# Performance work log

Measured on AMD Instinct MI355X. Metric: run time of the kernel, lower is better.

## Reference

```python
import jax, jax.numpy as jnp
import numpy as np
jax.config.update("jax_enable_x64", True)  # int64 hash codes for lattice keys

N_KPTS = 32768
C = 61      # feature channels; f-MLP input dim is C+3 = 64
D = 64      # disp-distribution channels
D_LAT = 8   # last f-layer output -> permutohedral position dim

# large odd 62-bit multipliers for the lattice-key hash (wraps mod 2^64)
_MULTS = np.array([2654435761405764093, 1181783497276652981,
                   3202034522624059733, 2685821657736338717,
                   1876998521354586173, 1481765933965188213,
                   2549297995355413921, 3373259426345127233], dtype=np.int64)


def _hcode(k, mults):
    return jnp.sum(k.astype(jnp.int64) * mults, axis=-1)


def _pl_filter(pos, vals):
    """Permutohedral lattice splat -> blur -> slice (approx. Gaussian filter).
    pos: (N, d) float32 lattice positions, vals: (N, vd) float32 values."""
    N, d = pos.shape
    vd = vals.shape[1]
    M = N * (d + 1)  # fixed-size hash table (every point touches d+1 vertices)
    # --- elevate onto hyperplane H_d in R^{d+1} ---
    scale = np.float32(np.sqrt(2.0 / 3.0) * (d + 1)) / np.sqrt(
        np.arange(1, d + 1, dtype=np.float32) * np.arange(2, d + 2, dtype=np.float32))
    E = np.zeros((d + 1, d), dtype=np.float32)
    E[0, :] = 1.0
    for i in range(1, d + 1):
        E[i, i - 1] = -float(i)
        E[i, i:] = 1.0
    elevated = (pos * jnp.asarray(scale, jnp.float32)) @ jnp.asarray(E).T  # (N, d+1)
    # --- nearest zero-colored lattice point and simplex ranks ---
    rem0 = jnp.floor(elevated / (d + 1) + 0.5) * (d + 1)
    sum_val = jnp.round(jnp.sum(rem0, -1) / (d + 1)).astype(jnp.int32)
    diff = elevated - rem0
    rank = jnp.argsort(jnp.argsort(-diff, axis=-1), axis=-1).astype(jnp.int32) + sum_val[:, None]
    lo = rank < 0
    hi = rank > d
    rem0 = rem0 + jnp.where(lo, float(d + 1), 0.0) - jnp.where(hi, float(d + 1), 0.0)
    rank = rank + jnp.where(lo, d + 1, 0) - jnp.where(hi, d + 1, 0)
    # --- barycentric coordinates ---
    t = (elevated - rem0) / (d + 1)
    rows = jnp.arange(N)[:, None]
    bary = jnp.zeros((N, d + 2), jnp.float32)
    bary = bary.at[rows, d - rank].add(t)
    bary = bary.at[rows, d + 1 - rank].add(-t)
    bary = bary.at[:, 0].add(1.0 + bary[:, d + 1])
    w = bary[:, :d + 1]  # (N, d+1) vertex weights
    # --- simplex vertex keys (first d coords; full key sums to 0) ---
    canonical = np.zeros((d + 1, d + 1), np.int32)
    for r in range(d + 1):
        canonical[r, :d + 1 - r] = r
        canonical[r, d + 1 - r:] = r - (d + 1)
    keys = rem0.astype(jnp.int32)[None, :, :d] + jnp.asarray(canonical)[:, rank[:, :d]]  # (d+1,N,d)
    # --- hash table via sorted unique codes (jit-safe fixed size) ---
    mults = jnp.asarray(_MULTS[:d])
    codes = _hcode(keys, mults).reshape(M)
    uniq, inv = jnp.unique(codes, return_inverse=True, size=M,
                           fill_value=jnp.iinfo(jnp.int64).max)
    inv = inv.reshape(M)
    # --- splat ---
    wv = (w.T[:, :, None] * vals[None]).reshape(M, vd)
    lat = jax.ops.segment_sum(wv, inv, num_segments=M)  # (M, vd)
    occ = jax.ops.segment_sum(jnp.ones((M,), jnp.float32), inv, num_segments=M) > 0
    ukeys = jnp.zeros((M, d), jnp.int32).at[inv].set(keys.reshape(M, d))
    # --- blur along each of the d+1 lattice directions ---
    for j in range(d + 1):
        off = np.ones(d + 1, np.int32)
        off[j] = -d
        o = jnp.asarray(off[:d])
        def _nbr(sign, lat=lat):
            c = _hcode(ukeys + sign * o, mults)
            i = jnp.clip(jnp.searchsorted(uniq, c), 0, M - 1)
            ok = (jnp.take(uniq, i) == c) & jnp.take(occ, i)
            return jnp.where(ok[:, None], jnp.take(lat, i, axis=0), 0.0)
        lat = jnp.where(occ[:, None], 0.5 * lat + 0.25 * (_nbr(1) + _nbr(-1)), lat)
    # --- slice ---
    alpha = 1.0 / (1.0 + 2.0 ** (-d))
    return jnp.sum(w.T[:, :, None] * jnp.take(lat, inv, axis=0).reshape(d + 1, N, vd), 0) * alpha


def _layernorm2(x, g, b):
    # LayerNorm(normalized_shape=(N, K)): stats over the last TWO dims jointly
    mu = jnp.mean(x, axis=(-2, -1), keepdims=True)
    var = jnp.mean((x - mu) ** 2, axis=(-2, -1), keepdims=True)
    return (x - mu) * jax.lax.rsqrt(var + 1e-5) * g + b


def setup_inputs() -> dict:
    key = jax.random.key(0)
    ks = jax.random.split(key, 16)
    f32 = jnp.float32
    rn = lambda k, shape, s=1.0: jax.random.normal(k, shape, dtype=f32) * s
    inp = {
        "kpts": rn(ks[0], (1, N_KPTS, 3)),
        "disps_distr": rn(ks[1], (1, N_KPTS, D)),
        "feats": rn(ks[2], (1, N_KPTS, C)),
    }
    i = 3
    for b in range(2):
        inp[f"Wd{b}0"] = rn(ks[i], (D, D), 0.05); i += 1
        inp[f"bd{b}0"] = jnp.zeros((D,), f32)
        inp[f"Wd{b}1"] = rn(ks[i], (D, D), 0.05); i += 1
        inp[f"bd{b}1"] = jnp.zeros((D,), f32)
        inp[f"Wf{b}"] = rn(ks[i], (C + 3, D_LAT), 0.1); i += 1
        inp[f"bf{b}"] = jnp.zeros((D_LAT,), f32)
        inp[f"g{b}"] = jnp.ones((N_KPTS, D_LAT), f32)
        inp[f"be{b}"] = jnp.zeros((N_KPTS, D_LAT), f32)
    return inp


def reference(kpts, disps_distr, feats, Wd00, bd00, Wd01, bd01, Wf0, bf0, g0, be0,
              Wd10, bd10, Wd11, bd11, Wf1, bf1, g1, be1):
    fk = jnp.concatenate([kpts, feats], axis=-1)  # (1, N, C+3)
    x = jnp.reshape(disps_distr, (1, N_KPTS, -1))
    blocks = [(Wd00, bd00, Wd01, bd01, Wf0, bf0, g0, be0),
              (Wd10, bd10, Wd11, bd11, Wf1, bf1, g1, be1)]
    for (Wd0, bd0, Wd1, bd1, Wf, bf, g, be) in blocks:
        x = jax.nn.relu(x @ Wd0 + bd0)   # d-layer 0
        x = jax.nn.relu(x @ Wd1 + bd1)   # d-layer 1
        # only the LAST f-layer output is used by the torch code (feats_kpts is never updated)
        pos = _layernorm2(jax.nn.relu(fk @ Wf + bf), g, be)  # (1, N, 8)
        x = _pl_filter(pos[0], x[0])[None]
    return x
```

## Files before the change

### kernel.cpp

```cpp
#include <hip/hip_runtime.h>
#include <hip/hip_bf16.h>
#include <hip/hip_fp16.h>
#include <stdint.h>

typedef unsigned long long u64;

#define NK 32768
#define DL 8
#define DP1 9
#define MT (NK*DP1)
#define HBITS 19
#define HSIZE (1u<<HBITS)
#define HMASK (HSIZE-1)
#define EMPTY_CODE 0xFFFFFFFFFFFFFFFFULL
#define NBLK 1152
#define HBLK (HSIZE/256)
#define CAP 32
#define MAXHUB 16384

#define MLPB 512
#define POSB (NK/32)
#define EMBB (NK/256)
#define HZB  384
#define VZB  128
#define NBRB (9*MT/256)
#define SPAB (MT/8)
#define SPBB 1152

__device__ __constant__ u64 c_mults[8] = {
    2654435761405764093ULL, 1181783497276652981ULL, 3202034522624059733ULL,
    2685821657736338717ULL, 1876998521354586173ULL, 1481765933965188213ULL,
    2549297995355413921ULL, 3373259426345127233ULL};

__device__ __forceinline__ unsigned int hmix(u64 x) {
    return (unsigned int)(x >> (64 - HBITS)) & HMASK;
}

__device__ __forceinline__ u64 dir_delta(int j) {
    u64 s = 0;
    #pragma unroll
    for (int k = 0; k < 8; k++) s += c_mults[k];
    return (j == 8) ? s : (s - 9ULL * c_mults[j]);
}

__device__ __forceinline__ float ldf(const void* p, int i, int bf) {
    if (bf) return __bfloat162float(((const __hip_bfloat16*)p)[i]);
    return ((const float*)p)[i];
}

__device__ __forceinline__ float bf2f(unsigned short u) {
    union { unsigned u; float f; } c; c.u = ((unsigned)u) << 16; return c.f;
}

__device__ __forceinline__ float4 ld4(const void* p, int vi, int bf) {
    if (bf) {
        ushort4 u = ((const ushort4*)p)[vi];
        float4 r;
        r.x = bf2f(u.x); r.y = bf2f(u.y); r.z = bf2f(u.z); r.w = bf2f(u.w);
        return r;
    }
    return ((const float4*)p)[vi];
}

__device__ __forceinline__ float rdlane(float v, int k) {
    return __uint_as_float(__builtin_amdgcn_readlane(__float_as_uint(v), k));
}

__global__ void k_detect(const unsigned* __restrict__ g0w, int* __restrict__ flag,
                         double* __restrict__ stats) {
    if (threadIdx.x == 0) {
        int f = 1;
        for (int i = 0; i < 8; i++) if (g0w[i] != 0x3F803F80u) f = 0;
        *flag = f;
        stats[0] = 0.0; stats[1] = 0.0;
    }
}

__global__ __launch_bounds__(256) void k_mlppos(const void* __restrict__ xin, int use_df_in,
    const void* __restrict__ W0, const void* __restrict__ B0,
    const void* __restrict__ W1, const void* __restrict__ B1,
    float* __restrict__ xout, const int* __restrict__ df,
    const void* __restrict__ kpts, const void* __restrict__ feats,
    const void* __restrict__ Wf, const void* __restrict__ Bf,
    float* __restrict__ pos_pre, double* __restrict__ stats) {
    __shared__ union {
        struct { float w0[4096], w1[4096]; } m;
        struct { float wf[512]; float fk[32][65]; float red[256], red2[256]; } p;
    } sm;
    int bf = *df;
    int tid = threadIdx.x;
    if (blockIdx.x < MLPB) {
        int bfin = use_df_in ? bf : 0;
        for (int i = tid; i < 1024; i += 256) {
            ((float4*)sm.m.w0)[i] = ld4(W0, i, bf);
            ((float4*)sm.m.w1)[i] = ld4(W1, i, bf);
        }
        __syncthreads();
        int lane = tid & 63, wv = tid >> 6;
        float b0c = ldf(B0, lane, bf);
        float b1c = ldf(B1, lane, bf);
        for (int t = 0; t < 2; t++) {
            int row0 = (blockIdx.x * 2 + t) * 32 + wv * 8;
            float a[8], acc[8];
            #pragma unroll
            for (int r = 0; r < 8; r++) {
                a[r] = ldf(xin, (row0 + r) * 64 + lane, bfin);
                acc[r] = b0c;
            }
            #pragma unroll 8
            for (int k = 0; k < 64; k++) {
                float w = sm.m.w0[k * 64 + lane];
                #pragma unroll
                for (int r = 0; r < 8; r++)
                    acc[r] = fmaf(rdlane(a[r], k), w, acc[r]);
            }
            #pragma unroll
            for (int r = 0; r < 8; r++) { a[r] = fmaxf(acc[r], 0.f); acc[r] = b1c; }
            #pragma unroll 8
            for (int k = 0; k < 64; k++) {
                float w = sm.m.w1[k * 64 + lane];
                #pragma unroll
                for (int r = 0; r < 8; r++)
                    acc[r] = fmaf(rdlane(a[r], k), w, acc[r]);
            }
            #pragma unroll
            for (int r = 0; r < 8; r++)
                xout[(row0 + r) * 64 + lane] = fmaxf(acc[r], 0.f);
        }
    } else {
        int n0 = (blockIdx.x - MLPB) * 32;
        for (int i = tid; i < 512; i += 256) sm.p.wf[i] = ldf(Wf, i, bf);
        for (int i = tid; i < 32*64; i += 256) {
            int pt = i >> 6, k = i & 63, n = n0 + pt;
            sm.p.fk[pt][k] = (k < 3) ? ldf(kpts, n*3 + k, bf) : ldf(feats, n*61 + (k-3), bf);
        }
        __syncthreads();
        int pt = tid >> 3, j = tid & 7, n = n0 + pt;
        float acc = ldf(Bf, j, bf);
        #pragma unroll
        for (int k = 0; k < 64; k++) acc = fmaf(sm.p.fk[pt][k], sm.p.wf[k*8+j], acc);
        acc = fmaxf(acc, 0.f);
        pos_pre[n*8 + j] = acc;
        sm.p.red[tid] = acc; sm.p.red2[tid] = acc * acc;
        __syncthreads();
        for (int s = 128; s > 0; s >>= 1) {
            if (tid < s) { sm.p.red[tid] += sm.p.red[tid+s]; sm.p.red2[tid] += sm.p.red2[tid+s]; }
            __syncthreads();
        }
        if (tid == 0) { atomicAdd(&stats[0], (double)sm.p.red[0]); atomicAdd(&stats[1], (double)sm.p.red2[0]); }
    }
}

__global__ __launch_bounds__(256) void k_embedz(const float* __restrict__ pos_pre,
    const double* __restrict__ stats, const void* __restrict__ g,
    const void* __restrict__ be, float* __restrict__ wgt,
    u64* __restrict__ pcodes, int* __restrict__ cnt, int* __restrict__ cnt2,
    int* __restrict__ hubid, const int* __restrict__ df,
    u64* __restrict__ htabc, float* __restrict__ hubval) {
    int bid = blockIdx.x;
    if (bid >= EMBB) {
        if (bid < EMBB + HZB) {
            uint4 f; f.x = 0xFFFFFFFFu; f.y = 0xFFFFFFFFu; f.z = 0xFFFFFFFFu; f.w = 0xFFFFFFFFu;
            for (int i = (bid - EMBB) * 256 + threadIdx.x; i < (int)(HSIZE/2); i += HZB * 256)
                ((uint4*)htabc)[i] = f;
        } else {
            uint4 z; z.x = 0; z.y = 0; z.z = 0; z.w = 0;
            for (int i = (bid - EMBB - HZB) * 256 + threadIdx.x; i < MAXHUB*16; i += VZB * 256)
                ((uint4*)hubval)[i] = z;
        }
        return;
    }
    int bf = *df;
    int n = bid * 256 + threadIdx.x;
    if (n >= NK) return;
    const double inv_cnt = 1.0 / (double)(NK * DL);
    double mud = stats[0] * inv_cnt;
    double vard = stats[1] * inv_cnt - mud * mud;
    float mu = (float)mud;
    float rs = rsqrtf((float)vard + 1e-5f);
    const float scale[8] = {
        5.196152422706632f, 3.0f, 2.1213203435596424f, 1.643167672515498f,
        1.3416407864998738f, 1.1338934190276817f, 0.9819805060619657f, 0.8660254037844386f};
    float c[8];
    #pragma unroll
    for (int k = 0; k < 8; k++) {
        float v = pos_pre[n*8 + k];
        float p = (v - mu) * rs * ldf(g, n*8 + k, bf) + ldf(be, n*8 + k, bf);
        c[k] = p * scale[k];
    }
    float sufa[9]; sufa[8] = 0.f;
    #pragma unroll
    for (int k = 7; k >= 0; k--) sufa[k] = sufa[k+1] + c[k];
    float elev[9];
    elev[0] = sufa[0];
    #pragma unroll
    for (int i = 1; i < 9; i++) elev[i] = sufa[i] - (float)i * c[i-1];
    int ri[9], sumv = 0;
    float diff[9];
    #pragma unroll
    for (int i = 0; i < 9; i++) {
        ri[i] = (int)floorf(elev[i] / 9.0f + 0.5f);
        sumv += ri[i];
        diff[i] = elev[i] - 9.f * (float)ri[i];
    }
    int rank[9];
    #pragma unroll
    for (int i = 0; i < 9; i++) {
        int r = 0;
        #pragma unroll
        for (int j = 0; j < 9; j++)
            r += (diff[j] > diff[i]) || ((diff[j] == diff[i]) && (j < i));
        rank[i] = r + sumv;
    }
    #pragma unroll
    for (int i = 0; i < 9; i++) {
        if (rank[i] < 0)      { rank[i] += 9; ri[i] += 1; }
        else if (rank[i] > 8) { rank[i] -= 9; ri[i] -= 1; }
    }
    float t[9];
    #pragma unroll
    for (int i = 0; i < 9; i++) t[i] = (elev[i] - 9.f * (float)ri[i]) / 9.f;
    float bary[10];
    #pragma unroll
    for (int i = 0; i < 10; i++) bary[i] = 0.f;
    #pragma unroll
    for (int i = 0; i < 9; i++) { bary[8 - rank[i]] += t[i]; bary[9 - rank[i]] -= t[i]; }
    bary[0] += 1.f + bary[9];
    for (int r = 0; r < 9; r++) {
        u64 code = 0;
        #pragma unroll
        for (int k = 0; k < 8; k++) {
            int key = 9 * ri[k] + ((rank[k] <= 8 - r) ? r : (r - 9));
            code += (u64)(long long)key * c_mults[k];
        }
        int m = n * 9 + r;
        wgt[m] = bary[r];
        pcodes[m] = code;
        cnt[m] = 0;
        cnt2[m] = 0;
        hubid[m] = -1;
    }
}

__global__ __launch_bounds__(256) void k_insert(const u64* __restrict__ pcodes,
    u64* __restrict__ htab_code, unsigned int* __restrict__ ppos) {
    int m = blockIdx.x * 256 + threadIdx.x;
    if (m >= MT) return;
    u64 code = pcodes[m];
    unsigned int pos = hmix(code);
    for (;;) {
        u64 cc = htab_code[pos];
        if (cc == code) break;
        if (cc == EMPTY_CODE) {
            u64 old = atomicCAS(&htab_code[pos], EMPTY_CODE, code);
            if (old == EMPTY_CODE || old == code) break;
        }
        pos = (pos + 1) & HMASK;
    }
    ppos[m] = pos;
}

__global__ __launch_bounds__(256) void k_occ(const u64* __restrict__ htab_code,
    int* __restrict__ bocc) {
    __shared__ int wcnt[4];
    unsigned int i = blockIdx.x * 256 + threadIdx.x;
    bool occ = (htab_code[i] != EMPTY_CODE);
    u64 mask = __ballot(occ);
    int lane = threadIdx.x & 63;
    if (lane == 0) wcnt[threadIdx.x >> 6] = __popcll(mask);
    __syncthreads();
    if (threadIdx.x == 0) bocc[blockIdx.x] = wcnt[0] + wcnt[1] + wcnt[2] + wcnt[3];
}

__global__ __launch_bounds__(256) void k_occscan(int* __restrict__ bocc,
    int* __restrict__ counter, int* __restrict__ nhub) {
    __shared__ int s[256];
    __shared__ int carry;
    int t = threadIdx.x;
    if (t == 0) { carry = 0; *nhub = 0; }
    __syncthreads();
    for (int c = 0; c < HBLK / 256; c++) {
        int i = c * 256 + t;
        int v = bocc[i];
        s[t] = v; __syncthreads();
        for (int off = 1; off < 256; off <<= 1) {
            int a = (t >= off) ? s[t-off] : 0;
            __syncthreads();
            s[t] += a;
            __syncthreads();
        }
        int cl = carry;
        bocc[i] = s[t] - v + cl;
        __syncthreads();
        if (t == 0) carry = cl + s[255];
        __syncthreads();
    }
    if (t == 0) *counter = carry;
}

__global__ __launch_bounds__(256) void k_assign2(const u64* __restrict__ htab_code,
    const int* __restrict__ bocc, int* __restrict__ htab_slot,
    u64* __restrict__ slot_code) {
    __shared__ int wbase[4];
    unsigned int i = blockIdx.x * 256 + threadIdx.x;
    u64 cde = htab_code[i];
    bool occ = (cde != EMPTY_CODE);
    int lane = threadIdx.x & 63;
    int wid  = threadIdx.x >> 6;
    u64 mask = __ballot(occ);
    int prefix = __popcll(mask & ((1ULL << lane) - 1ULL));
    if (lane == 0) wbase[wid] = __popcll(mask);
    __syncthreads();
    if (threadIdx.x == 0) {
        int run = bocc[blockIdx.x];
        for (int w = 0; w < 4; w++) { int c = wbase[w]; wbase[w] = run; run += c; }
    }
    __syncthreads();
    if (occ) {
        int s = wbase[wid] + prefix;
        htab_slot[i] = s;
        slot_code[s] = cde;
    }
}

__global__ __launch_bounds__(256) void k_nbrlookup(const u64* __restrict__ slot_code,
    const u64* __restrict__ htab_code, const int* __restrict__ htab_slot,
    const int* __restrict__ counter, int2* __restrict__ nbr,
    const unsigned int* __restrict__ ppos, int* __restrict__ sidx,
    int* __restrict__ cnt) {
    if (blockIdx.x < NBRB) {
        int idx = blockIdx.x * 256 + threadIdx.x;
        int j = idx / MT;
        int sl = idx - j * MT;
        int count = *counter;
        if (sl >= count) return;
        u64 dj = dir_delta(j);
        u64 code = slot_code[sl];
        int res[2];
        #pragma unroll
        for (int s = 0; s < 2; s++) {
            u64 cde = code + (s ? (u64)(0ULL - dj) : dj);
            unsigned int pos = hmix(cde);
            int r = -1;
            for (;;) {
                u64 cc = htab_code[pos];
                if (cc == cde) { r = htab_slot[pos]; break; }
                if (cc == EMPTY_CODE) break;
                pos = (pos + 1) & HMASK;
            }
            res[s] = r;
        }
        nbr[j * MT + sl] = make_int2(res[0], res[1]);
    } else {
        int m = (blockIdx.x - NBRB) * 256 + threadIdx.x;
        if (m >= MT) return;
        int s = htab_slot[ppos[m]];
        sidx[m] = s;
        atomicAdd(&cnt[s], 1);
    }
}

__global__ __launch_bounds__(256) void k_scan1(const int* __restrict__ cnt,
    int* __restrict__ exbuf, int* __restrict__ bsum,
    int* __restrict__ hublist, int* __restrict__ hubid, int* __restrict__ nhub) {
    __shared__ int s[256];
    int t = threadIdx.x;
    int i = blockIdx.x * 256 + t;
    int v = cnt[i];
    if (v > CAP) {
        int h = atomicAdd(nhub, 1);
        if (h < MAXHUB) { hublist[h] = i; hubid[i] = h; }
    }
    s[t] = v; __syncthreads();
    for (int off = 1; off < 256; off <<= 1) {
        int a = (t >= off) ? s[t-off] : 0;
        __syncthreads();
        s[t] += a;
        __syncthreads();
    }
    exbuf[i] = s[t] - v;
    if (t == 255) bsum[blockIdx.x] = s[255];
}

__global__ __launch_bounds__(256) void k_scan2(int* __restrict__ bsum) {
    __shared__ int s[256];
    __shared__ int carry;
    int t = threadIdx.x;
    if (t == 0) carry = 0;
    __syncthreads();
    for (int c = 0; c < (NBLK + 255) / 256; c++) {
        int i = c * 256 + t;
        int v = (i < NBLK) ? bsum[i] : 0;
        s[t] = v; __syncthreads();
        for (int off = 1; off < 256; off <<= 1) {
            int a = (t >= off) ? s[t-off] : 0;
            __syncthreads();
            s[t] += a;
            __syncthreads();
        }
        int cl = carry;
        if (i < NBLK) bsum[i] = s[t] - v + cl;
        __syncthreads();
        if (t == 0) carry = cl + s[255];
        __syncthreads();
    }
}

__global__ __launch_bounds__(256) void k_scatter(const int* __restrict__ sidx,
    const int* __restrict__ exbuf, const int* __restrict__ bsum,
    int* __restrict__ cnt2, int* __restrict__ list) {
    int m = blockIdx.x * 256 + threadIdx.x;
    if (m < MT) {
        int s = sidx[m];
        int ofs = atomicAdd(&cnt2[s], 1);
        list[exbuf[s] + bsum[s >> 8] + ofs] = m;
    }
}

__global__ __launch_bounds__(256) void k_splat(const float* __restrict__ xbuf,
    const float* __restrict__ wgt, const int* __restrict__ exbuf,
    const int* __restrict__ bsum, const int* __restrict__ cnt,
    const int* __restrict__ list, __half* __restrict__ val,
    const int* __restrict__ counter, const int* __restrict__ sidx,
    const int* __restrict__ hubid, float* __restrict__ hubval) {
    const float2* x2 = (const float2*)xbuf;
    int lane = threadIdx.x & 31;
    if (blockIdx.x < SPAB) {
        int count = *counter;
        int sl = blockIdx.x * 8 + (threadIdx.x >> 5);
        if (sl >= count) return;
        int c = cnt[sl];
        if (c > CAP) return;
        int st = exbuf[sl] + bsum[sl >> 8];
        float2 acc = make_float2(0.f, 0.f);
        int mm = 0; float ww = 0.f;
        if (lane < c) { mm = list[st + lane]; ww = wgt[mm]; }
        for (int k = 0; k < c; k++) {
            int   m = __shfl(mm, k, 32);
            float w = __shfl(ww, k, 32);
            float2 xv = x2[(m / 9) * 32 + lane];
            acc.x = fmaf(w, xv.x, acc.x);
            acc.y = fmaf(w, xv.y, acc.y);
        }
        ((__half2*)val)[(size_t)sl * 32 + lane] = __float22half2_rn(acc);
    } else {
        int chunk = (blockIdx.x - SPAB) * 8 + (threadIdx.x >> 5);
        int e = chunk * 32 + lane;
        int m = 0, hid = -1; float w = 0.f; int hub = 0;
        if (e < MT) {
            m = list[e];
            int slot = sidx[m];
            hub = (cnt[slot] > CAP);
            if (hub) { w = wgt[m]; hid = hubid[slot]; }
        }
        u64 bal = __ballot(hub);
        unsigned int half = (threadIdx.x & 32) ? (unsigned int)(bal >> 32) : (unsigned int)bal;
        if (!half) return;
        float2 acc = make_float2(0.f, 0.f);
        int cur = -1;
        while (half) {
            int k = __ffs(half) - 1; half &= half - 1;
            int   hk = __shfl(hid, k, 32);
            int   mk = __shfl(m, k, 32);
            float wk = __shfl(w, k, 32);
            float2 xv = x2[(mk / 9) * 32 + lane];
            if (hk != cur) {
                if (cur >= 0) {
                    atomicAdd(&hubval[(size_t)cur * 64 + 2*lane    ], acc.x);
                    atomicAdd(&hubval[(size_t)cur * 64 + 2*lane + 1], acc.y);
                }
                cur = hk; acc = make_float2(0.f, 0.f);
            }
            acc.x = fmaf(wk, xv.x, acc.x);
            acc.y = fmaf(wk, xv.y, acc.y);
        }
        atomicAdd(&hubval[(size_t)cur * 64 + 2*lane    ], acc.x);
        atomicAdd(&hubval[(size_t)cur * 64 + 2*lane + 1], acc.y);
    }
}

__global__ __launch_bounds__(256) void k_hubcvt(const float* __restrict__ hubval,
    const int* __restrict__ hublist, const int* __restrict__ nhub,
    __half* __restrict__ val) {
    int idx = blockIdx.x * 256 + threadIdx.x;
    int hi = idx >> 5, lane = idx & 31;
    if (hi >= *nhub) return;
    int sl = hublist[hi];
    float2 v = ((const float2*)hubval)[(size_t)hi * 32 + lane];
    ((__half2*)val)[(size_t)sl * 32 + lane] = __float22half2_rn(v);
}

__global__ __launch_bounds__(256) void k_blur(const __half* __restrict__ vin,
    __half* __restrict__ vout, const int2* __restrict__ nbrj,
    const int* __restrict__ counter) {
    int idx = blockIdx.x * 256 + threadIdx.x;
    int sl = idx >> 3, lane = idx & 7;
    int count = *counter;
    if (sl >= count) return;
    int2 nbp = nbrj[sl];
    typedef union { uint4 u; __half2 h[4]; } row16;
    const uint4* vin4 = (const uint4*)vin;
    uint4* vout4 = (uint4*)vout;
    row16 S, A, B, O;
    S.u = vin4[(size_t)sl*8 + lane];
    uint4 z; z.x = 0; z.y = 0; z.z = 0; z.w = 0;
    A.u = (nbp.x >= 0) ? vin4[(size_t)nbp.x*8 + lane] : z;
    B.u = (nbp.y >= 0) ? vin4[(size_t)nbp.y*8 + lane] : z;
    #pragma unroll
    for (int k = 0; k < 4; k++) {
        float2 fs = __half22float2(S.h[k]);
        float2 fa = __half22float2(A.h[k]);
        float2 fb = __half22float2(B.h[k]);
        float2 r;
        r.x = 0.5f * fs.x + 0.25f * (fa.x + fb.x);
        r.y = 0.5f * fs.y + 0.25f * (fa.y + fb.y);
        O.h[k] = __float22half2_rn(r);
    }
    vout4[(size_t)sl*8 + lane] = O.u;
}

__global__ __launch_bounds__(256) void k_slice(const float* __restrict__ wgt,
    const int* __restrict__ sidx, const __half* __restrict__ val,
    float* __restrict__ outf, void* __restrict__ outb, int write_out,
    const int* __restrict__ df, double* __restrict__ stats) {
    int idx = blockIdx.x * 256 + threadIdx.x;
    if (idx == 0) { stats[0] = 0.0; stats[1] = 0.0; }
    if (idx >= NK * 32) return;
    int bf = *df;
    const __half2* v2 = (const __half2*)val;
    int n = idx >> 5, cp = idx & 31;
    float2 acc = make_float2(0.f, 0.f);
    #pragma unroll
    for (int r = 0; r < 9; r++) {
        int m = n * 9 + r;
        float w = wgt[m];
        float2 hv = __half22float2(v2[(size_t)sidx[m]*32 + cp]);
        acc.x = fmaf(w, hv.x, acc.x);
        acc.y = fmaf(w, hv.y, acc.y);
    }
    acc.x *= 0.9961089494163424f;
    acc.y *= 0.9961089494163424f;
    int o = n*64 + cp*2;
    if (write_out) {
        if (bf) {
            __hip_bfloat16* ob = (__hip_bfloat16*)outb;
            ob[o]   = __float2bfloat16(acc.x);
            ob[o+1] = __float2bfloat16(acc.y);
        } else {
            float* of = (float*)outb;
            of[o] = acc.x; of[o+1] = acc.y;
        }
    } else {
        outf[o] = acc.x; outf[o+1] = acc.y;
    }
}

extern "C" void kernel_launch(void* const* d_in, const int* in_sizes, int n_in,
                              void* d_out, int out_size, void* d_ws, size_t ws_size,
                              hipStream_t stream) {
    const void* kpts  = d_in[0];
    const void* disps = d_in[1];
    const void* feats = d_in[2];

    char* p = (char*)d_ws;
    float* xbuf     = (float*)p;  p += (size_t)NK*64*4;
    float* pos_pre  = (float*)p;  p += (size_t)NK*8*4;
    double* stats   = (double*)p; p += 256;
    int*   dflag    = (int*)p;    p += 256;
    float* wgt      = (float*)p;  p += (size_t)MT*4;
    int*   sidx     = (int*)p;    p += (size_t)MT*4;
    u64*   pcodes   = (u64*)p;    p += (size_t)MT*8;
    unsigned int* ppos = (unsigned int*)p; p += (size_t)MT*4;
    u64*   htabc    = (u64*)p;    p += (size_t)HSIZE*8;
    int*   htabs    = (int*)p;    p += (size_t)HSIZE*4;
    u64*   slotc    = (u64*)p;    p += (size_t)MT*8;
    int*   counter  = (int*)p;    p += 256;
    int*   nhub     = (int*)p;    p += 256;
    int*   bocc     = (int*)p;    p += (size_t)HBLK*4;
    int*   cnt      = (int*)p;    p += (size_t)MT*4;
    int*   cnt2     = (int*)p;    p += (size_t)MT*4;
    int*   hubid    = (int*)p;    p += (size_t)MT*4;
    int*   exbuf    = (int*)p;    p += (size_t)MT*4;
    int*   list     = (int*)p;    p += (size_t)MT*4;
    int*   bsum     = (int*)p;    p += 256*32;
    int*   hublist  = (int*)p;    p += (size_t)MAXHUB*4;
    float* hubval   = (float*)p;  p += (size_t)MAXHUB*64*4;
    int2*  nbr      = (int2*)p;   p += (size_t)MT*9*8;
    __half* valA    = (__half*)p; p += (size_t)MT*64*2;
    __half* valB    = (__half*)p; p += (size_t)MT*64*2;

    k_detect<<<1, 64, 0, stream>>>((const unsigned*)d_in[3 + 6], dflag, stats);

    for (int b = 0; b < 2; b++) {
        const void* W0 = d_in[3 + b*8 + 0];
        const void* B0 = d_in[3 + b*8 + 1];
        const void* W1 = d_in[3 + b*8 + 2];
        const void* B1 = d_in[3 + b*8 + 3];
        const void* Wf = d_in[3 + b*8 + 4];
        const void* Bf = d_in[3 + b*8 + 5];
        const void* G  = d_in[3 + b*8 + 6];
        const void* Be = d_in[3 + b*8 + 7];

        k_mlppos<<<MLPB + POSB, 256, 0, stream>>>(
            b == 0 ? disps : (const void*)xbuf, b == 0 ? 1 : 0,
            W0, B0, W1, B1, xbuf, dflag,
            kpts, feats, Wf, Bf, pos_pre, stats);

        k_embedz<<<EMBB + HZB + VZB, 256, 0, stream>>>(pos_pre, stats, G, Be, wgt,
                                                       pcodes, cnt, cnt2, hubid, dflag,
                                                       htabc, hubval);
        k_insert<<<NBLK, 256, 0, stream>>>(pcodes, htabc, ppos);
        k_occ<<<HBLK, 256, 0, stream>>>(htabc, bocc);
        k_occscan<<<1, 256, 0, stream>>>(bocc, counter, nhub);
        k_assign2<<<HBLK, 256, 0, stream>>>(htabc, bocc, htabs, slotc);
        k_nbrlookup<<<NBRB + NBLK, 256, 0, stream>>>(slotc, htabc, htabs, counter, nbr,
                                                     ppos, sidx, cnt);

        k_scan1<<<NBLK, 256, 0, stream>>>(cnt, exbuf, bsum, hublist, hubid, nhub);
        k_scan2<<<1, 256, 0, stream>>>(bsum);
        k_scatter<<<NBLK, 256, 0, stream>>>(sidx, exbuf, bsum, cnt2, list);
        k_splat<<<SPAB + SPBB, 256, 0, stream>>>(xbuf, wgt, exbuf, bsum, cnt, list,
                                                 valA, counter, sidx, hubid, hubval);
        k_hubcvt<<<(MAXHUB*32)/256, 256, 0, stream>>>(hubval, hublist, nhub, valA);

        for (int j = 0; j < 9; j++) {
            const __half* vin = (j & 1) ? valB : valA;
            __half*       vout = (j & 1) ? valA : valB;
            k_blur<<<(MT*8 + 255)/256, 256, 0, stream>>>(vin, vout, nbr + (size_t)j*MT, counter);
        }
        k_slice<<<(NK*64)/256, 256, 0, stream>>>(wgt, sidx, valB, xbuf,
                                                 d_out, b == 1 ? 1 : 0, dflag, stats);
    }
}
```

Before: 710.4 us.

## Register-tile the disparity MLP and split it from the position kernel

The fused MLP/position kernel is split into two launches. The MLP now stages a 64-row input tile in shared memory, and each thread computes 32 output channels for one row using float4 weight reads. This replaces the old scheme, where each lane produced one channel for 8 rows via readlane broadcasts. The aim is more FMAs per shared-memory load and no scalar readlane serialization, at the cost of more registers and shared memory per block, an extra launch, and losing the concurrency the fused grid gave the MLP and position blocks.

```diff
diff --git a/kernel.cpp b/kernel.cpp
--- a/kernel.cpp
+++ b/kernel.cpp
@@ -18,7 +18,7 @@
 #define CAP 32
 #define MAXHUB 16384
 
-#define MLPB 512
+#define MLPGRID (NK/64)
 #define POSB (NK/32)
 #define EMBB (NK/256)
 #define HZB  384
@@ -62,10 +62,6 @@
     return ((const float4*)p)[vi];
 }
 
-__device__ __forceinline__ float rdlane(float v, int k) {
-    return __uint_as_float(__builtin_amdgcn_readlane(__float_as_uint(v), k));
-}
-
 __global__ void k_detect(const unsigned* __restrict__ g0w, int* __restrict__ flag,
                          double* __restrict__ stats) {
     if (threadIdx.x == 0) {
@@ -76,79 +72,102 @@
     }
 }
 
-__global__ __launch_bounds__(256) void k_mlppos(const void* __restrict__ xin, int use_df_in,
+__global__ __launch_bounds__(128) void k_mlp(const void* __restrict__ xin, int use_df_in,
     const void* __restrict__ W0, const void* __restrict__ B0,
     const void* __restrict__ W1, const void* __restrict__ B1,
-    float* __restrict__ xout, const int* __restrict__ df,
-    const void* __restrict__ kpts, const void* __restrict__ feats,
-    const void* __restrict__ Wf, const void* __restrict__ Bf,
-    float* __restrict__ pos_pre, double* __restrict__ stats) {
-    __shared__ union {
-        struct { float w0[4096], w1[4096]; } m;
-        struct { float wf[512]; float fk[32][65]; float red[256], red2[256]; } p;
-    } sm;
+    float* __restrict__ xout, const int* __restrict__ df) {
+    __shared__ float ws0[4096], ws1[4096];
+    __shared__ float xs[64][65];
+    int bf = *df;
+    int bfin = use_df_in ? bf : 0;
+    int tid = threadIdx.x;
+    int lane = tid & 63, wv = tid >> 6;
+    int row0 = blockIdx.x * 64;
+    for (int i = tid; i < 4096; i += 128) {
+        ws0[i] = ldf(W0, i, bf);
+        ws1[i] = ldf(W1, i, bf);
+    }
+    for (int i = tid; i < 1024; i += 128) {
+        int r = i >> 4, kv = i & 15;
+        float4 v = ld4(xin, (row0 + r) * 16 + kv, bfin);
+        xs[r][kv*4  ] = v.x; xs[r][kv*4+1] = v.y;
+        xs[r][kv*4+2] = v.z; xs[r][kv*4+3] = v.w;
+    }
+    __syncthreads();
+    int c0 = wv * 32;
+    float acc[32];
+    #pragma unroll
+    for (int c = 0; c < 32; c++) acc[c] = ldf(B0, c0 + c, bf);
+    for (int k = 0; k < 64; k++) {
+        float xv = xs[lane][k];
+        #pragma unroll
+        for (int c4 = 0; c4 < 8; c4++) {
+            float4 w = *(const float4*)&ws0[k*64 + c0 + c4*4];
+            acc[c4*4  ] = fmaf(xv, w.x, acc[c4*4  ]);
+            acc[c4*4+1] = fmaf(xv, w.y, acc[c4*4+1]);
+            acc[c4*4+2] = fmaf(xv, w.z, acc[c4*4+2]);
+            acc[c4*4+3] = fmaf(xv, w.w, acc[c4*4+3]);
+        }
+    }
+    #pragma unroll
+    for (int c = 0; c < 32; c++) acc[c] = fmaxf(acc[c], 0.f);
+    __syncthreads();
+    #pragma unroll
+    for (int c = 0; c < 32; c++) xs[lane][c0 + c] = acc[c];
+    __syncthreads();
+    #pragma unroll
+    for (int c = 0; c < 32; c++) acc[c] = ldf(B1, c0 + c, bf);
+    for (int k = 0; k < 64; k++) {
+        float xv = xs[lane][k];
+        #pragma unroll
+        for (int c4 = 0; c4 < 8; c4++) {
+            float4 w = *(const float4*)&ws1[k*64 + c0 + c4*4];
+            acc[c4*4  ] = fmaf(xv, w.x, acc[c4*4  ]);
+            acc[c4*4+1] = fmaf(xv, w.y, acc[c4*4+1]);
+            acc[c4*4+2] = fmaf(xv, w.z, acc[c4*4+2]);
+            acc[c4*4+3] = fmaf(xv, w.w, acc[c4*4+3]);
+        }
+    }
+    #pragma unroll
+    for (int c4 = 0; c4 < 8; c4++) {
+        float4 o;
+        o.x = fmaxf(acc[c4*4  ], 0.f);
+        o.y = fmaxf(acc[c4*4+1], 0.f);
+        o.z = fmaxf(acc[c4*4+2], 0.f);
+        o.w = fmaxf(acc[c4*4+3], 0.f);
+        *(float4*)&xout[(row0 + lane)*64 + c0 + c4*4] = o;
+    }
+}
+
+__global__ __launch_bounds__(256) void k_pos(const void* __restrict__ kpts,
+    const void* __restrict__ feats, const void* __restrict__ Wf,
+    const void* __restrict__ Bf, float* __restrict__ pos_pre,
+    double* __restrict__ stats, const int* __restrict__ df) {
+    __shared__ float wf[64*8];
+    __shared__ float fk[32][65];
+    __shared__ float red[256], red2[256];
     int bf = *df;
     int tid = threadIdx.x;
-    if (blockIdx.x < MLPB) {
-        int bfin = use_df_in ? bf : 0;
-        for (int i = tid; i < 1024; i += 256) {
-            ((float4*)sm.m.w0)[i] = ld4(W0, i, bf);
-            ((float4*)sm.m.w1)[i] = ld4(W1, i, bf);
-        }
+    int n0 = blockIdx.x * 32;
+    for (int i = tid; i < 512; i += 256) wf[i] = ldf(Wf, i, bf);
+    for (int i = tid; i < 32*64; i += 256) {
+        int pt = i >> 6, k = i & 63, n = n0 + pt;
+        fk[pt][k] = (k < 3) ? ldf(kpts, n*3 + k, bf) : ldf(feats, n*61 + (k-3), bf);
+    }
+    __syncthreads();
+    int pt = tid >> 3, j = tid & 7, n = n0 + pt;
+    float acc = ldf(Bf, j, bf);
+    #pragma unroll
+    for (int k = 0; k < 64; k++) acc = fmaf(fk[pt][k], wf[k*8+j], acc);
+    acc = fmaxf(acc, 0.f);
+    pos_pre[n*8 + j] = acc;
+    red[tid] = acc; red2[tid] = acc * acc;
+    __syncthreads();
+    for (int s = 128; s > 0; s >>= 1) {
+        if (tid < s) { red[tid] += red[tid+s]; red2[tid] += red2[tid+s]; }
         __syncthreads();
-        int lane = tid & 63, wv = tid >> 6;
-        float b0c = ldf(B0, lane, bf);
-        float b1c = ldf(B1, lane, bf);
-        for (int t = 0; t < 2; t++) {
-            int row0 = (blockIdx.x * 2 + t) * 32 + wv * 8;
-            float a[8], acc[8];
-            #pragma unroll
-            for (int r = 0; r < 8; r++) {
-                a[r] = ldf(xin, (row0 + r) * 64 + lane, bfin);
-                acc[r] = b0c;
-            }
-            #pragma unroll 8
-            for (int k = 0; k < 64; k++) {
-                float w = sm.m.w0[k * 64 + lane];
-                #pragma unroll
-                for (int r = 0; r < 8; r++)
-                    acc[r] = fmaf(rdlane(a[r], k), w, acc[r]);
-            }
-            #pragma unroll
-            for (int r = 0; r < 8; r++) { a[r] = fmaxf(acc[r], 0.f); acc[r] = b1c; }
-            #pragma unroll 8
-            for (int k = 0; k < 64; k++) {
-                float w = sm.m.w1[k * 64 + lane];
-                #pragma unroll
-                for (int r = 0; r < 8; r++)
-                    acc[r] = fmaf(rdlane(a[r], k), w, acc[r]);
-            }
-            #pragma unroll
-            for (int r = 0; r < 8; r++)
-                xout[(row0 + r) * 64 + lane] = fmaxf(acc[r], 0.f);
-        }
-    } else {
-        int n0 = (blockIdx.x - MLPB) * 32;
-        for (int i = tid; i < 512; i += 256) sm.p.wf[i] = ldf(Wf, i, bf);
-        for (int i = tid; i < 32*64; i += 256) {
-            int pt = i >> 6, k = i & 63, n = n0 + pt;
-            sm.p.fk[pt][k] = (k < 3) ? ldf(kpts, n*3 + k, bf) : ldf(feats, n*61 + (k-3), bf);
-        }
-        __syncthreads();
-        int pt = tid >> 3, j = tid & 7, n = n0 + pt;
-        float acc = ldf(Bf, j, bf);
-        #pragma unroll
-        for (int k = 0; k < 64; k++) acc = fmaf(sm.p.fk[pt][k], sm.p.wf[k*8+j], acc);
-        acc = fmaxf(acc, 0.f);
-        pos_pre[n*8 + j] = acc;
-        sm.p.red[tid] = acc; sm.p.red2[tid] = acc * acc;
-        __syncthreads();
-        for (int s = 128; s > 0; s >>= 1) {
-            if (tid < s) { sm.p.red[tid] += sm.p.red[tid+s]; sm.p.red2[tid] += sm.p.red2[tid+s]; }
-            __syncthreads();
-        }
-        if (tid == 0) { atomicAdd(&stats[0], (double)sm.p.red[0]); atomicAdd(&stats[1], (double)sm.p.red2[0]); }
-    }
+    }
+    if (tid == 0) { atomicAdd(&stats[0], (double)red[0]); atomicAdd(&stats[1], (double)red2[0]); }
 }
 
 __global__ __launch_bounds__(256) void k_embedz(const float* __restrict__ pos_pre,
@@ -601,10 +620,10 @@
         const void* G  = d_in[3 + b*8 + 6];
         const void* Be = d_in[3 + b*8 + 7];
 
-        k_mlppos<<<MLPB + POSB, 256, 0, stream>>>(
+        k_mlp<<<MLPGRID, 128, 0, stream>>>(
             b == 0 ? disps : (const void*)xbuf, b == 0 ? 1 : 0,
-            W0, B0, W1, B1, xbuf, dflag,
-            kpts, feats, Wf, Bf, pos_pre, stats);
+            W0, B0, W1, B1, xbuf, dflag);
+        k_pos<<<POSB, 256, 0, stream>>>(kpts, feats, Wf, Bf, pos_pre, stats, dflag);
 
         k_embedz<<<EMBB + HZB + VZB, 256, 0, stream>>>(pos_pre, stats, G, Be, wgt,
                                                        pcodes, cnt, cnt2, hubid, dflag,
```

After: 762.7 us. 7.4% more time.
